# Kernel optimization log

Measured on AMD Instinct MI355X. Metric: run time of the kernel, lower is better.

Reference implementation:

```python
import jax, jax.numpy as jnp
import numpy as np

B, N, F, H = 4, 2048, 1024, 16
D = F // H  # head dim = 64


def setup_inputs() -> dict:
    key = jax.random.key(0)
    ks = jax.random.split(key, 7)
    s = 1.0 / np.sqrt(F)
    return {
        "x": jax.random.normal(ks[0], (B, N, F), dtype=jnp.float32),
        "Wq": jax.random.normal(ks[1], (F, F), dtype=jnp.float32) * s,
        "bq": jnp.zeros((F,), dtype=jnp.float32),
        "Wk": jax.random.normal(ks[2], (F, F), dtype=jnp.float32) * s,
        "bk": jnp.zeros((F,), dtype=jnp.float32),
        "Wv": jax.random.normal(ks[3], (F, F), dtype=jnp.float32) * s,
        "bv": jnp.zeros((F,), dtype=jnp.float32),
    }


def reference(x, Wq, bq, Wk, bk, Wv, bv):
    # Q/K/V projections (nn.Dense: x @ W + b)
    q = x @ Wq + bq
    k = x @ Wk + bk
    v = x @ Wv + bv
    # split heads: b n (h d) -> b h n d
    split = lambda t: t.reshape(B, N, H, D).transpose(0, 2, 1, 3)
    q, k, v = split(q), split(k), split(v)
    scale = jnp.asarray(np.sqrt(D), dtype=x.dtype)
    # scores: [B, H, N, N]
    scores = jnp.einsum("bhnd,bhmd->bhnm", q, k) / scale
    # additive causal mask (tril): masked positions set to dtype min
    causal = jnp.tril(jnp.ones((N, N), dtype=bool))
    dmin = jnp.finfo(scores.dtype).min
    scores = jnp.where(causal[None, None], scores, dmin)
    attn = jax.nn.softmax(scores, axis=-1)
    out = jnp.einsum("bhnm,bhmd->bhnd", attn, v)
    # merge heads: b h n d -> b n (h d)
    return out.transpose(0, 2, 1, 3).reshape(B, N, F)
```

## Files before the change

kernel.cpp:

```cpp
#include <hip/hip_runtime.h>

#define LOG2E 1.44269504088896340736f

typedef float f32x4 __attribute__((ext_vector_type(4)));
typedef float f32x16 __attribute__((ext_vector_type(16)));
typedef __bf16 bf16x8 __attribute__((ext_vector_type(8)));

__device__ __forceinline__ unsigned short f2bf(float f){
  unsigned int u = __builtin_bit_cast(unsigned int, f);
  u += 0x7fffu + ((u >> 16) & 1u);
  return (unsigned short)(u >> 16);
}

__device__ __forceinline__ void gload_lds16(const void* g, void* l){
  __builtin_amdgcn_global_load_lds(
      (const __attribute__((address_space(1))) unsigned int*)g,
      (__attribute__((address_space(3))) unsigned int*)l, 16, 0, 0);
}

__global__ __launch_bounds__(256) void cvt_x(const float* __restrict__ x,
                                             unsigned short* __restrict__ xs){
  int t = blockIdx.x * 256 + threadIdx.x;
  int m = t >> 7, c = t & 127;
  const float4* p = (const float4*)(x + ((size_t)m << 10) + (c << 3));
  float4 f0 = p[0], f1 = p[1];
  unsigned int w0 = f2bf(f0.x) | ((unsigned int)f2bf(f0.y) << 16);
  unsigned int w1 = f2bf(f0.z) | ((unsigned int)f2bf(f0.w) << 16);
  unsigned int w2 = f2bf(f1.x) | ((unsigned int)f2bf(f1.y) << 16);
  unsigned int w3 = f2bf(f1.z) | ((unsigned int)f2bf(f1.w) << 16);
  int byte = (c << 4) ^ ((m & 7) << 4);
  *(uint4*)((char*)xs + ((size_t)m << 11) + byte) = make_uint4(w0, w1, w2, w3);
}

__global__ __launch_bounds__(256) void cvt_w(const float* __restrict__ Wq,
                                             const float* __restrict__ Wk,
                                             const float* __restrict__ Wv,
                                             unsigned short* __restrict__ wtq,
                                             unsigned short* __restrict__ wtk,
                                             unsigned short* __restrict__ wtv){
  int t = blockIdx.x * 256 + threadIdx.x;
  int n = t & 1023, c = t >> 10;
  const float* W = blockIdx.y == 0 ? Wq : blockIdx.y == 1 ? Wk : Wv;
  unsigned short* o = blockIdx.y == 0 ? wtq : blockIdx.y == 1 ? wtk : wtv;
  unsigned int w[4];
  #pragma unroll
  for (int i = 0; i < 4; ++i){
    float a = W[(size_t)(c * 8 + 2 * i) * 1024 + n];
    float b = W[(size_t)(c * 8 + 2 * i + 1) * 1024 + n];
    w[i] = f2bf(a) | ((unsigned int)f2bf(b) << 16);
  }
  int byte = (c << 4) ^ ((n & 7) << 4);
  *(uint4*)((char*)o + ((size_t)n << 11) + byte) = make_uint4(w[0], w[1], w[2], w[3]);
}

__global__ __launch_bounds__(256) void proj_gemm(
    const unsigned short* __restrict__ xs,
    const unsigned short* __restrict__ wt0, const unsigned short* __restrict__ wt1,
    const unsigned short* __restrict__ wt2,
    const float* __restrict__ b0, const float* __restrict__ b1, const float* __restrict__ b2,
    unsigned short* __restrict__ o0, unsigned short* __restrict__ o1,
    unsigned short* __restrict__ o2){
  __shared__ char As[16384];
  __shared__ char Bs[16384];
  const int v = blockIdx.z;
  const unsigned short* wt = v == 0 ? wt0 : v == 1 ? wt1 : wt2;
  const float* bias = v == 0 ? b0 : v == 1 ? b1 : b2;
  const int row0 = blockIdx.x << 7;
  const int col0 = blockIdx.y << 7;
  const int tid = threadIdx.x;
  const int wave = tid >> 6, lane = tid & 63;
  const int wr = wave >> 1, wc = wave & 1;
  f32x4 acc[4][4] = {};

  const char* abase = (const char*)xs + (size_t)(row0 + wave * 8 + (lane >> 3)) * 2048 + ((lane & 7) << 4);
  const char* bbase = (const char*)wt + (size_t)(col0 + wave * 8 + (lane >> 3)) * 2048 + ((lane & 7) << 4);
  char* aldst = As + wave * 1024;
  char* bldst = Bs + wave * 1024;

  for (int kk = 0; kk < 16; ++kk){
    const size_t koff = (size_t)kk << 7;
    #pragma unroll
    for (int c = 0; c < 4; ++c){
      gload_lds16(abase + (size_t)c * 65536 + koff, aldst + c * 4096);
      gload_lds16(bbase + (size_t)c * 65536 + koff, bldst + c * 4096);
    }
    __syncthreads();
    #pragma unroll
    for (int s = 0; s < 2; ++s){
      bf16x8 af[4], bfr[4];
      #pragma unroll
      for (int mt = 0; mt < 4; ++mt){
        int r = wr * 64 + mt * 16 + (lane & 15);
        int byte = (((lane >> 4) << 4) + (s << 6)) ^ ((r & 7) << 4);
        af[mt] = *(const bf16x8*)(As + r * 128 + byte);
      }
      #pragma unroll
      for (int nt = 0; nt < 4; ++nt){
        int cc = wc * 64 + nt * 16 + (lane & 15);
        int byte = (((lane >> 4) << 4) + (s << 6)) ^ ((cc & 7) << 4);
        bfr[nt] = *(const bf16x8*)(Bs + cc * 128 + byte);
      }
      #pragma unroll
      for (int mt = 0; mt < 4; ++mt)
        #pragma unroll
        for (int nt = 0; nt < 4; ++nt)
          acc[mt][nt] = __builtin_amdgcn_mfma_f32_16x16x32_bf16(af[mt], bfr[nt], acc[mt][nt], 0, 0, 0);
    }
    __syncthreads();
  }

  #pragma unroll
  for (int nt = 0; nt < 4; ++nt){
    int col = col0 + wc * 64 + nt * 16 + (lane & 15);
    float bia = bias[col];
    int h = col >> 6, d = col & 63;
    #pragma unroll
    for (int mt = 0; mt < 4; ++mt){
      #pragma unroll
      for (int r = 0; r < 4; ++r){
        int mrow = row0 + wr * 64 + mt * 16 + ((lane >> 4) << 2) + r;
        int b = mrow >> 11, n = mrow & 2047;
        float val = acc[mt][nt][r] + bia;
        if (v == 0){
          o0[((size_t)((b * 16 + h) * 2048 + n) << 6) + d] = f2bf(val * 0.125f);
        } else if (v == 1){
          o1[((size_t)((b * 16 + h) * 2048 + n) << 6) + d] = f2bf(val);
        } else {
          o2[((size_t)((b * 16 + h) * 64 + d) << 11) + n] = f2bf(val);
        }
      }
    }
  }
}

template<int NKB, bool DIAG>
__device__ __forceinline__ void attn_tile_lds(
    const char* __restrict__ Kl, const char* __restrict__ Vl,
    int l31, int hi, int sw,
    const bf16x8* qf, float& m_, float& l_, f32x16& o0, f32x16& o1)
{
  bf16x8 kf0[4], kf1[4];
  #pragma unroll
  for (int i = 0; i < 4; ++i)
    kf0[i] = *(const bf16x8*)(Kl + l31 * 128 + ((((2 * i + hi) << 4)) ^ sw));
  if (NKB == 2){
    #pragma unroll
    for (int i = 0; i < 4; ++i)
      kf1[i] = *(const bf16x8*)(Kl + (32 + l31) * 128 + ((((2 * i + hi) << 4)) ^ sw));
  }
  f32x16 s0 = {}, s1 = {};
  #pragma unroll
  for (int i = 0; i < 4; ++i)
    s0 = __builtin_amdgcn_mfma_f32_32x32x16_bf16(kf0[i], qf[i], s0, 0, 0, 0);
  if (NKB == 2){
    #pragma unroll
    for (int i = 0; i < 4; ++i)
      s1 = __builtin_amdgcn_mfma_f32_32x32x16_bf16(kf1[i], qf[i], s1, 0, 0, 0);
  }
  bf16x8 vf0[NKB * 2], vf1[NKB * 2];
  #pragma unroll
  for (int ks = 0; ks < NKB * 2; ++ks){
    vf0[ks] = *(const bf16x8*)(Vl + l31 * 128 + ((((2 * ks + hi) << 4)) ^ sw));
    vf1[ks] = *(const bf16x8*)(Vl + (32 + l31) * 128 + ((((2 * ks + hi) << 4)) ^ sw));
  }
  if (DIAG){
    const int hi4 = hi * 4;
    #pragma unroll
    for (int r = 0; r < 16; ++r){
      int kloc = (r & 3) + 8 * (r >> 2) + hi4;
      if (NKB == 1){ if (kloc > l31) s0[r] = -1e38f; }
      else         { if (kloc > l31) s1[r] = -1e38f; }
    }
  }
  float mloc = -1e38f;
  #pragma unroll
  for (int r = 0; r < 16; ++r){
    mloc = fmaxf(mloc, s0[r]);
    if (NKB == 2) mloc = fmaxf(mloc, s1[r]);
  }
  mloc = fmaxf(mloc, __shfl_xor(mloc, 32));
  const float mnew = fmaxf(m_, mloc);
  const float mc = mnew * LOG2E;
  const float corr = __builtin_amdgcn_exp2f(__builtin_fmaf(m_, LOG2E, -mc));
  m_ = mnew;
  float rs = 0.f;
  #pragma unroll
  for (int r = 0; r < 16; ++r){
    s0[r] = __builtin_amdgcn_exp2f(__builtin_fmaf(s0[r], LOG2E, -mc));
    rs += s0[r];
    if (NKB == 2){
      s1[r] = __builtin_amdgcn_exp2f(__builtin_fmaf(s1[r], LOG2E, -mc));
      rs += s1[r];
    }
  }
  rs += __shfl_xor(rs, 32);
  l_ = l_ * corr + rs;
  o0 *= corr; o1 *= corr;
  unsigned int u0[NKB * 4], u1[NKB * 4];
  #pragma unroll
  for (int c = 0; c < NKB * 4; ++c){
    const int b4 = (c & 3) * 4;
    float p0 = (c < 4) ? s0[b4]     : s1[b4];
    float p1 = (c < 4) ? s0[b4 + 1] : s1[b4 + 1];
    float p2 = (c < 4) ? s0[b4 + 2] : s1[b4 + 2];
    float p3 = (c < 4) ? s0[b4 + 3] : s1[b4 + 3];
    unsigned int w0, w1;
    asm("v_cvt_pk_bf16_f32 %0, %1, %2" : "=v"(w0) : "v"(p0), "v"(p1));
    asm("v_cvt_pk_bf16_f32 %0, %1, %2" : "=v"(w1) : "v"(p2), "v"(p3));
    u0[c] = w0; u1[c] = w1;
  }
  #pragma unroll
  for (int ks = 0; ks < NKB * 2; ++ks){
    unsigned int a0 = u0[2 * ks], b0 = u0[2 * ks + 1];
    unsigned int a1 = u1[2 * ks], b1 = u1[2 * ks + 1];
    asm("v_permlane32_swap_b32 %0, %1" : "+v"(a0), "+v"(b0));
    asm("v_permlane32_swap_b32 %0, %1" : "+v"(a1), "+v"(b1));
    union { unsigned int u[4]; bf16x8 v; } pa;
    pa.u[0] = a0; pa.u[1] = a1; pa.u[2] = b0; pa.u[3] = b1;
    o0 = __builtin_amdgcn_mfma_f32_32x32x16_bf16(vf0[ks], pa.v, o0, 0, 0, 0);
    o1 = __builtin_amdgcn_mfma_f32_32x32x16_bf16(vf1[ks], pa.v, o1, 0, 0, 0);
  }
}

__global__ __launch_bounds__(256) void attn(
    const unsigned short* __restrict__ Qg, const unsigned short* __restrict__ Kg,
    const unsigned short* __restrict__ Vt, float* __restrict__ out){
  const int bid = blockIdx.x;
  const int xcd = bid & 7, slot = bid >> 3;
  const int head = xcd * 8 + (slot & 7);
  const int u = 15 - (slot >> 3);
  const int wave = threadIdx.x >> 6, lane = threadIdx.x & 63;
  const int l31 = lane & 31, hi = lane >> 5;
  const int sw = (l31 & 7) << 4;
  const int t = 4 * u + wave;
  const int q0 = t * 32;
  const int nfull = t >> 1;
  const bool odd = t & 1;
  const int ktmax = 2 * u + 1;

  const unsigned short* qb = Qg + ((size_t)head << 17);
  const char* kbg = (const char*)(Kg + ((size_t)head << 17));
  const char* vbg = (const char*)(Vt + ((size_t)head << 17));

  __shared__ char Kl[2][8192];
  __shared__ char Vl[2][8192];

  bf16x8 qf[4];
  #pragma unroll
  for (int i = 0; i < 4; ++i)
    qf[i] = *(const bf16x8*)(qb + (size_t)(q0 + l31) * 64 + i * 16 + hi * 8);

  const int csw = (((lane & 7) ^ (lane >> 3)) << 4) ;
  const int lrow = lane >> 3;
  #define STAGE(buf, kt) do {                                                   \
    _Pragma("unroll")                                                           \
    for (int r_ = 0; r_ < 2; ++r_){                                             \
      int rows8_ = (r_ * 4 + wave) * 8;                                         \
      int row_ = rows8_ + lrow;                                                 \
      gload_lds16(kbg + (size_t)((kt) * 64 + row_) * 128 + csw,                 \
                  Kl[buf] + (r_ * 4 + wave) * 1024);                            \
      gload_lds16(vbg + (size_t)row_ * 4096 + (size_t)(kt) * 128 + csw,         \
                  Vl[buf] + (r_ * 4 + wave) * 1024);                            \
    }                                                                           \
  } while (0)

  float m_ = -1e38f, l_ = 0.f;
  f32x16 o0 = {}, o1 = {};

  STAGE(0, 0);
  __syncthreads();
  int cur = 0;
  for (int kt = 0; kt <= ktmax; ++kt){
    if (kt < ktmax) STAGE(cur ^ 1, kt + 1);
    if (kt < nfull){
      attn_tile_lds<2, false>(Kl[cur], Vl[cur], l31, hi, sw, qf, m_, l_, o0, o1);
    } else if (kt == nfull){
      if (odd) attn_tile_lds<2, true>(Kl[cur], Vl[cur], l31, hi, sw, qf, m_, l_, o0, o1);
      else     attn_tile_lds<1, true>(Kl[cur], Vl[cur], l31, hi, sw, qf, m_, l_, o0, o1);
    }
    __syncthreads();
    cur ^= 1;
  }
  #undef STAGE

  const float inv = 1.f / l_;
  const int b = head >> 4, h = head & 15;
  float* op = out + ((size_t)(b * 2048 + q0 + l31) << 10) + h * 64 + hi * 4;
  #pragma unroll
  for (int c = 0; c < 4; ++c){
    *(float4*)(op + 8 * c) =
        make_float4(o0[4*c]*inv, o0[4*c+1]*inv, o0[4*c+2]*inv, o0[4*c+3]*inv);
    *(float4*)(op + 32 + 8 * c) =
        make_float4(o1[4*c]*inv, o1[4*c+1]*inv, o1[4*c+2]*inv, o1[4*c+3]*inv);
  }
}

extern "C" void kernel_launch(void* const* d_in, const int* in_sizes, int n_in,
                              void* d_out, int out_size, void* d_ws, size_t ws_size,
                              hipStream_t stream){
  const float* x  = (const float*)d_in[0];
  const float* Wq = (const float*)d_in[1];
  const float* bq = (const float*)d_in[2];
  const float* Wk = (const float*)d_in[3];
  const float* bk = (const float*)d_in[4];
  const float* Wv = (const float*)d_in[5];
  const float* bv = (const float*)d_in[6];
  float* out = (float*)d_out;
  char* ws = (char*)d_ws;
  unsigned short* xs  = (unsigned short*)(ws);
  unsigned short* wtq = (unsigned short*)(ws + 16777216);
  unsigned short* wtk = (unsigned short*)(ws + 18874368);
  unsigned short* wtv = (unsigned short*)(ws + 20971520);
  unsigned short* Qg  = (unsigned short*)(ws + 23068672);
  unsigned short* Kg  = (unsigned short*)(ws + 39845888);
  unsigned short* Vt  = (unsigned short*)(ws + 56623104);

  cvt_x<<<4096, 256, 0, stream>>>(x, xs);
  cvt_w<<<dim3(512, 3), 256, 0, stream>>>(Wq, Wk, Wv, wtq, wtk, wtv);
  proj_gemm<<<dim3(64, 8, 3), 256, 0, stream>>>(xs, wtq, wtk, wtv, bq, bk, bv, Qg, Kg, Vt);
  attn<<<1024, 256, 0, stream>>>(Qg, Kg, Vt, out);
}
```

Measured before the change: 243.9 us.

## Rewrite projection GEMM as 256x256 tile, 8-wave, multi-stage pipelined kernel

The QKV projection GEMM moves from 128x128 tiles with 4 waves and a single-buffered LDS loop to 256x256 tiles with 8 waves. It uses four LDS slots for A and for B, staged in half-tiles, with global-to-LDS prefetch interleaved between MFMA phases, explicit vmcnt/lgkmcnt waits and s_setprio around the MFMA blocks. The aim is to hide global load latency and improve operand reuse per block. In exchange the grid shrinks to 384 blocks, 128 KB of LDS is needed per block, and the barrier choreography is fragile.

```diff
diff --git a/kernel.cpp b/kernel.cpp
--- a/kernel.cpp
+++ b/kernel.cpp
@@ -53,72 +53,157 @@
   *(uint4*)((char*)o + ((size_t)n << 11) + byte) = make_uint4(w[0], w[1], w[2], w[3]);
 }
 
-__global__ __launch_bounds__(256) void proj_gemm(
+__global__ __launch_bounds__(512, 2) void proj_gemm(
     const unsigned short* __restrict__ xs,
     const unsigned short* __restrict__ wt0, const unsigned short* __restrict__ wt1,
     const unsigned short* __restrict__ wt2,
     const float* __restrict__ b0, const float* __restrict__ b1, const float* __restrict__ b2,
     unsigned short* __restrict__ o0, unsigned short* __restrict__ o1,
     unsigned short* __restrict__ o2){
-  __shared__ char As[16384];
-  __shared__ char Bs[16384];
+  __shared__ char AL[4][16384];
+  __shared__ char BL[4][16384];
   const int v = blockIdx.z;
   const unsigned short* wt = v == 0 ? wt0 : v == 1 ? wt1 : wt2;
   const float* bias = v == 0 ? b0 : v == 1 ? b1 : b2;
-  const int row0 = blockIdx.x << 7;
-  const int col0 = blockIdx.y << 7;
+  const int row0 = blockIdx.x << 8;
+  const int col0 = blockIdx.y << 8;
   const int tid = threadIdx.x;
   const int wave = tid >> 6, lane = tid & 63;
-  const int wr = wave >> 1, wc = wave & 1;
-  f32x4 acc[4][4] = {};
-
-  const char* abase = (const char*)xs + (size_t)(row0 + wave * 8 + (lane >> 3)) * 2048 + ((lane & 7) << 4);
-  const char* bbase = (const char*)wt + (size_t)(col0 + wave * 8 + (lane >> 3)) * 2048 + ((lane & 7) << 4);
-  char* aldst = As + wave * 1024;
-  char* bldst = Bs + wave * 1024;
-
-  for (int kk = 0; kk < 16; ++kk){
-    const size_t koff = (size_t)kk << 7;
-    #pragma unroll
-    for (int c = 0; c < 4; ++c){
-      gload_lds16(abase + (size_t)c * 65536 + koff, aldst + c * 4096);
-      gload_lds16(bbase + (size_t)c * 65536 + koff, bldst + c * 4096);
-    }
-    __syncthreads();
-    #pragma unroll
-    for (int s = 0; s < 2; ++s){
-      bf16x8 af[4], bfr[4];
+  const int wr = wave >> 2, wc = wave & 3;
+  const int l15 = lane & 15, lg = lane >> 4;
+  const char* xsb = (const char*)xs;
+  const char* wtb = (const char*)wt;
+
+  f32x4 acc[8][4] = {};
+
+#define STAGE_A(slot, kt, half) do {                                          \
+  _Pragma("unroll")                                                           \
+  for (int j_ = 0; j_ < 2; ++j_){                                             \
+    int rh_ = (j_ * 8 + wave) * 8 + (lane >> 3);                              \
+    int gr_ = row0 + (half) * 128 + rh_;                                      \
+    gload_lds16(xsb + (size_t)gr_ * 2048 + (kt) * 128 + ((lane & 7) << 4),    \
+                AL[slot] + (j_ * 8 + wave) * 1024);                           \
+  } } while (0)
+
+#define STAGE_B(slot, kt, half) do {                                          \
+  _Pragma("unroll")                                                           \
+  for (int j_ = 0; j_ < 2; ++j_){                                             \
+    int rh_ = (j_ * 8 + wave) * 8 + (lane >> 3);                              \
+    int gc_ = col0 + (half) * 128 + rh_;                                      \
+    gload_lds16(wtb + (size_t)gc_ * 2048 + (kt) * 128 + ((lane & 7) << 4),    \
+                BL[slot] + (j_ * 8 + wave) * 1024);                           \
+  } } while (0)
+
+  STAGE_A(0, 0, 0); STAGE_A(1, 0, 1); STAGE_B(0, 0, 0); STAGE_B(1, 0, 1);
+  STAGE_B(2, 1, 0); STAGE_A(2, 1, 0);
+  asm volatile("s_waitcnt vmcnt(4)" ::: "memory");
+  __builtin_amdgcn_s_barrier();
+
+  const int fb0 = ((lg    ) ^ (l15 & 7)) << 4;
+  const int fb1 = ((lg + 4) ^ (l15 & 7)) << 4;
+  const int browB = (wc & 1) << 6;
+
+  for (int w = 0; w < 16; ++w){
+    const int par  = (w & 1) << 1;
+    const int npar = 2 - par;
+    const char* Asl = AL[par + wr];
+    const char* Bsl = BL[par + (wc >> 1)];
+    bf16x8 afr[4][2], bfA[2][2], bfB[2][2];
+
+    #pragma unroll
+    for (int mt = 0; mt < 4; ++mt){
+      afr[mt][0] = *(const bf16x8*)(Asl + (mt * 16 + l15) * 128 + fb0);
+      afr[mt][1] = *(const bf16x8*)(Asl + (mt * 16 + l15) * 128 + fb1);
+    }
+    #pragma unroll
+    for (int nt = 0; nt < 2; ++nt){
+      bfA[nt][0] = *(const bf16x8*)(Bsl + (browB + nt * 16 + l15) * 128 + fb0);
+      bfA[nt][1] = *(const bf16x8*)(Bsl + (browB + nt * 16 + l15) * 128 + fb1);
+    }
+    __builtin_amdgcn_sched_barrier(0);
+    if (w + 1 < 16){ STAGE_B(npar + 1, w + 1, 1); STAGE_A(npar + 1, w + 1, 1); }
+    __builtin_amdgcn_s_barrier();
+    asm volatile("s_waitcnt lgkmcnt(0)" ::: "memory");
+    __builtin_amdgcn_sched_barrier(0);
+    __builtin_amdgcn_s_setprio(1);
+    #pragma unroll
+    for (int mt = 0; mt < 4; ++mt)
       #pragma unroll
-      for (int mt = 0; mt < 4; ++mt){
-        int r = wr * 64 + mt * 16 + (lane & 15);
-        int byte = (((lane >> 4) << 4) + (s << 6)) ^ ((r & 7) << 4);
-        af[mt] = *(const bf16x8*)(As + r * 128 + byte);
+      for (int nt = 0; nt < 2; ++nt){
+        acc[mt][nt] = __builtin_amdgcn_mfma_f32_16x16x32_bf16(afr[mt][0], bfA[nt][0], acc[mt][nt], 0, 0, 0);
+        acc[mt][nt] = __builtin_amdgcn_mfma_f32_16x16x32_bf16(afr[mt][1], bfA[nt][1], acc[mt][nt], 0, 0, 0);
       }
+    __builtin_amdgcn_s_setprio(0);
+    __builtin_amdgcn_s_barrier();
+
+    #pragma unroll
+    for (int nt = 0; nt < 2; ++nt){
+      bfB[nt][0] = *(const bf16x8*)(Bsl + (browB + 32 + nt * 16 + l15) * 128 + fb0);
+      bfB[nt][1] = *(const bf16x8*)(Bsl + (browB + 32 + nt * 16 + l15) * 128 + fb1);
+    }
+    __builtin_amdgcn_s_barrier();
+    asm volatile("s_waitcnt lgkmcnt(0)" ::: "memory");
+    __builtin_amdgcn_sched_barrier(0);
+    __builtin_amdgcn_s_setprio(1);
+    #pragma unroll
+    for (int mt = 0; mt < 4; ++mt)
       #pragma unroll
-      for (int nt = 0; nt < 4; ++nt){
-        int cc = wc * 64 + nt * 16 + (lane & 15);
-        int byte = (((lane >> 4) << 4) + (s << 6)) ^ ((cc & 7) << 4);
-        bfr[nt] = *(const bf16x8*)(Bs + cc * 128 + byte);
+      for (int nt = 0; nt < 2; ++nt){
+        acc[mt][2 + nt] = __builtin_amdgcn_mfma_f32_16x16x32_bf16(afr[mt][0], bfB[nt][0], acc[mt][2 + nt], 0, 0, 0);
+        acc[mt][2 + nt] = __builtin_amdgcn_mfma_f32_16x16x32_bf16(afr[mt][1], bfB[nt][1], acc[mt][2 + nt], 0, 0, 0);
       }
+    __builtin_amdgcn_s_setprio(0);
+    __builtin_amdgcn_s_barrier();
+
+    #pragma unroll
+    for (int mt = 0; mt < 4; ++mt){
+      afr[mt][0] = *(const bf16x8*)(Asl + ((64 + mt * 16) + l15) * 128 + fb0);
+      afr[mt][1] = *(const bf16x8*)(Asl + ((64 + mt * 16) + l15) * 128 + fb1);
+    }
+    __builtin_amdgcn_sched_barrier(0);
+    if (w + 2 < 16) STAGE_B(par + 0, w + 2, 0);
+    __builtin_amdgcn_s_barrier();
+    asm volatile("s_waitcnt lgkmcnt(0)" ::: "memory");
+    __builtin_amdgcn_sched_barrier(0);
+    __builtin_amdgcn_s_setprio(1);
+    #pragma unroll
+    for (int mt = 0; mt < 4; ++mt)
       #pragma unroll
-      for (int mt = 0; mt < 4; ++mt)
-        #pragma unroll
-        for (int nt = 0; nt < 4; ++nt)
-          acc[mt][nt] = __builtin_amdgcn_mfma_f32_16x16x32_bf16(af[mt], bfr[nt], acc[mt][nt], 0, 0, 0);
-    }
-    __syncthreads();
-  }
+      for (int nt = 0; nt < 2; ++nt){
+        acc[4 + mt][nt] = __builtin_amdgcn_mfma_f32_16x16x32_bf16(afr[mt][0], bfA[nt][0], acc[4 + mt][nt], 0, 0, 0);
+        acc[4 + mt][nt] = __builtin_amdgcn_mfma_f32_16x16x32_bf16(afr[mt][1], bfA[nt][1], acc[4 + mt][nt], 0, 0, 0);
+      }
+    __builtin_amdgcn_s_setprio(0);
+    __builtin_amdgcn_s_barrier();
+
+    if (w + 2 < 16) STAGE_A(par + 0, w + 2, 0);
+    __builtin_amdgcn_s_barrier();
+    __builtin_amdgcn_s_setprio(1);
+    #pragma unroll
+    for (int mt = 0; mt < 4; ++mt)
+      #pragma unroll
+      for (int nt = 0; nt < 2; ++nt){
+        acc[4 + mt][2 + nt] = __builtin_amdgcn_mfma_f32_16x16x32_bf16(afr[mt][0], bfB[nt][0], acc[4 + mt][2 + nt], 0, 0, 0);
+        acc[4 + mt][2 + nt] = __builtin_amdgcn_mfma_f32_16x16x32_bf16(afr[mt][1], bfB[nt][1], acc[4 + mt][2 + nt], 0, 0, 0);
+      }
+    __builtin_amdgcn_s_setprio(0);
+    if (w >= 14) asm volatile("s_waitcnt vmcnt(0)" ::: "memory");
+    else         asm volatile("s_waitcnt vmcnt(4)" ::: "memory");
+    __builtin_amdgcn_s_barrier();
+  }
+#undef STAGE_A
+#undef STAGE_B
 
   #pragma unroll
   for (int nt = 0; nt < 4; ++nt){
-    int col = col0 + wc * 64 + nt * 16 + (lane & 15);
+    int col = col0 + wc * 64 + nt * 16 + l15;
     float bia = bias[col];
     int h = col >> 6, d = col & 63;
     #pragma unroll
-    for (int mt = 0; mt < 4; ++mt){
+    for (int mt = 0; mt < 8; ++mt){
       #pragma unroll
       for (int r = 0; r < 4; ++r){
-        int mrow = row0 + wr * 64 + mt * 16 + ((lane >> 4) << 2) + r;
+        int mrow = row0 + wr * 128 + mt * 16 + lg * 4 + r;
         int b = mrow >> 11, n = mrow & 2047;
         float val = acc[mt][nt][r] + bia;
         if (v == 0){
@@ -317,6 +402,6 @@
 
   cvt_x<<<4096, 256, 0, stream>>>(x, xs);
   cvt_w<<<dim3(512, 3), 256, 0, stream>>>(Wq, Wk, Wv, wtq, wtk, wtv);
-  proj_gemm<<<dim3(64, 8, 3), 256, 0, stream>>>(xs, wtq, wtk, wtv, bq, bk, bv, Qg, Kg, Vt);
+  proj_gemm<<<dim3(32, 4, 3), 512, 0, stream>>>(xs, wtq, wtk, wtv, bq, bk, bv, Qg, Kg, Vt);
   attn<<<1024, 256, 0, stream>>>(Qg, Kg, Vt, out);
 }
```

Result: slower. 257.4 us (+5.5%).
